# Performance work log

Measured on AMD Instinct MI355X. Metric: run time of the kernel, lower is better.

The kernel has to match this reference:

```python
import jax, jax.numpy as jnp
import numpy as np

D_MODEL = 1024
NUM_HEADS = 16
D_HEAD = 64
N_CTX = 2048
BATCH = 4
NEG_INF = -1e10  # matches torch masked_fill value


def setup_inputs() -> dict:
    key = jax.random.key(0)
    k1, k2, k3, k4, k5 = jax.random.split(key, 5)
    s = 1.0 / np.sqrt(D_MODEL).astype(np.float32)
    x = jax.random.normal(k1, (BATCH, N_CTX, D_MODEL), dtype=jnp.float32)
    W_K = jax.random.normal(k2, (NUM_HEADS, D_HEAD, D_MODEL), dtype=jnp.float32) * s
    W_Q = jax.random.normal(k3, (NUM_HEADS, D_HEAD, D_MODEL), dtype=jnp.float32) * s
    W_V = jax.random.normal(k4, (NUM_HEADS, D_HEAD, D_MODEL), dtype=jnp.float32) * s
    W_O = jax.random.normal(k5, (D_MODEL, NUM_HEADS * D_HEAD), dtype=jnp.float32) * s
    return {"x": x, "W_K": W_K, "W_Q": W_Q, "W_V": W_V, "W_O": W_O}


def reference(x, W_K, W_Q, W_V, W_O):
    b, q_len, d_model = x.shape
    d_head = W_K.shape[1]
    # projections: b=batch, p=pos, d=d_model, i=head, h=d_head
    K = jnp.einsum('bpd,ihd->biph', x, W_K)
    Q = jnp.einsum('bpd,ihd->biph', x, W_Q)
    V = jnp.einsum('bpd,ihd->biph', x, W_V)
    # scores[b, i, q, p] = Q[b,i,q,:] . K[b,i,p,:]
    scores = jnp.einsum('biph,biqh->biqp', K, Q)
    mask = jnp.tril(jnp.ones((q_len, q_len), dtype=bool))
    # NOTE: original masks with -1e10 BEFORE dividing by sqrt(d_head)
    scores = jnp.where(mask[None, None, :, :], scores, NEG_INF)
    attn = jax.nn.softmax(scores / np.sqrt(d_head).astype(np.float32), axis=-1)
    z = jnp.einsum('biph,biqp->biqh', V, attn)
    z_flat = jnp.transpose(z, (0, 2, 1, 3)).reshape(b, q_len, -1)  # b q (i h)
    out = jnp.einsum('bqf,df->bqd', z_flat, W_O)
    return out
```

## Files before the change

kernel.cpp:

```cpp
#include <hip/hip_runtime.h>
#include <hip/hip_bf16.h>


typedef short short8 __attribute__((ext_vector_type(8)));
typedef float f32x4 __attribute__((ext_vector_type(4)));

#define MFMA16(a, b, c) __builtin_amdgcn_mfma_f32_16x16x32_bf16((a), (b), (c), 0, 0, 0)

static __device__ __forceinline__ ushort f2bf(float f) {
  union { __hip_bfloat16 h; ushort u; } cv;
  cv.h = __float2bfloat16(f);
  return cv.u;
}

static __device__ __forceinline__ float fexp2(float x) {
#if __has_builtin(__builtin_amdgcn_exp2f)
  return __builtin_amdgcn_exp2f(x);
#else
  return __expf(x * 0.69314718056f);
#endif
}

static __device__ __forceinline__ void block_sync_lds() {
  asm volatile("s_waitcnt lgkmcnt(0)" ::: "memory");
  __builtin_amdgcn_s_barrier();
  __builtin_amdgcn_sched_barrier(0);
}

static __device__ __forceinline__ void block_sync_full() {
  asm volatile("s_waitcnt vmcnt(0) lgkmcnt(0)" ::: "memory");
  __builtin_amdgcn_s_barrier();
  __builtin_amdgcn_sched_barrier(0);
}

static __device__ __forceinline__ void store_out(float* p, float v) { *p = v; }
static __device__ __forceinline__ void store_out(__hip_bfloat16* p, float v) {
  *p = __float2bfloat16(v);
}

__global__ __launch_bounds__(256) void convert_all_kernel(
    const float* __restrict__ wq, const float* __restrict__ wk,
    const float* __restrict__ wv, const float* __restrict__ wo,
    const float* __restrict__ x, ushort* __restrict__ wqkv,
    ushort* __restrict__ wob, ushort* __restrict__ xb) {
  constexpr int W4 = 262144;
  constexpr size_t WSZ = (size_t)1024 * 1024;
  const int i = blockIdx.x * blockDim.x + threadIdx.x;
  const float* src;
  ushort* dst;
  int j;
  if (i < 2 * W4) {
    if (i < W4)      { src = wq; dst = wqkv;           j = i; }
    else             { src = wk; dst = wqkv + WSZ;     j = i - W4; }
  } else if (i < 4 * W4) {
    if (i < 3 * W4)  { src = wv; dst = wqkv + 2 * WSZ; j = i - 2 * W4; }
    else             { src = wo; dst = wob;            j = i - 3 * W4; }
  } else {
    src = x; dst = xb; j = i - 4 * W4;
  }
  const float4 v = ((const float4*)src)[j];
  ushort4 o;
  o.x = f2bf(v.x); o.y = f2bf(v.y); o.z = f2bf(v.z); o.w = f2bf(v.w);
  ((ushort4*)dst)[j] = o;
}

template <typename OUT_T>
__global__ __launch_bounds__(256) void gemm_kernel(
    const ushort* __restrict__ A, int lda, const ushort* __restrict__ B, int ldb,
    OUT_T* __restrict__ C, int ldc, int K, int cpx) {
  __shared__ __align__(16) ushort As[128 * 64];
  __shared__ __align__(16) ushort Bs[128 * 64];
  const int tid = threadIdx.x;
  const int wave = tid >> 6, lane = tid & 63;
  const int lm = lane & 15, quad = lane >> 4;

  const int id = blockIdx.x;
  const int local = id >> 3;
  const int nt = (id & 7) * cpx + local % cpx;
  const int mt = local / cpx;
  const size_t m0 = (size_t)mt * 128;
  const size_t n0 = (size_t)nt * 128;

  const int rl = lane >> 3;
  const int cs = (lane & 7) ^ rl;
  const int fsw = lm & 7;

  f32x4 acc[4][4] = {};
  for (int k0 = 0; k0 < K; k0 += 64) {
    __syncthreads();
#pragma unroll
    for (int j = 0; j < 4; ++j) {
      const int ch = wave * 4 + j;
      const ushort* gb = B + (n0 + ch * 8 + rl) * (size_t)ldb + k0 + cs * 8;
      __builtin_amdgcn_global_load_lds(
          (const __attribute__((address_space(1))) void*)gb,
          (__attribute__((address_space(3))) void*)(Bs + ch * 512), 16, 0, 0);
      const ushort* ga = A + (m0 + ch * 8 + rl) * (size_t)lda + k0 + cs * 8;
      __builtin_amdgcn_global_load_lds(
          (const __attribute__((address_space(1))) void*)ga,
          (__attribute__((address_space(3))) void*)(As + ch * 512), 16, 0, 0);
    }
    __syncthreads();

    const int wm = (wave >> 1) * 64, wn = (wave & 1) * 64;
#pragma unroll
    for (int ks = 0; ks < 2; ++ks) {
      short8 a[4], b[4];
#pragma unroll
      for (int i = 0; i < 4; ++i)
        a[i] = *(const short8*)(As + (wm + i * 16 + lm) * 64 +
                                ((((ks * 4 + quad) ^ fsw) & 7) << 3));
#pragma unroll
      for (int j = 0; j < 4; ++j)
        b[j] = *(const short8*)(Bs + (wn + j * 16 + lm) * 64 +
                                ((((ks * 4 + quad) ^ fsw) & 7) << 3));
#pragma unroll
      for (int i = 0; i < 4; ++i)
#pragma unroll
        for (int j = 0; j < 4; ++j)
          acc[i][j] = MFMA16(a[i], b[j], acc[i][j]);
    }
  }

  const int wm = (wave >> 1) * 64, wn = (wave & 1) * 64;
  const int rq = quad * 4;
#pragma unroll
  for (int i = 0; i < 4; ++i)
#pragma unroll
    for (int j = 0; j < 4; ++j)
#pragma unroll
      for (int r = 0; r < 4; ++r)
        store_out(&C[(m0 + wm + i * 16 + rq + r) * (size_t)ldc + n0 + wn + j * 16 + lm],
                  acc[i][j][r]);
}

static __device__ __forceinline__ void vt_write8(ushort* vtbuf, int h0, int hsw,
                                                 int p, const short8& v) {
  const int pc = (p >> 3) ^ hsw;
  ushort* row = vtbuf + h0 * 64 + (p & 7);
#pragma unroll
  for (int u = 0; u < 8; ++u)
    row[u * 64 + (((pc ^ u) & 7) << 3)] = ((const ushort*)&v)[u];
}

static __device__ __forceinline__ void stage_k(const ushort* kglob, int pbase,
                                               ushort* kbuf, int wave, int lane) {
  const int rl = lane >> 3;
  const int c = (lane & 7) ^ rl;
#pragma unroll
  for (int j = 0; j < 2; ++j) {
    const int ch = wave * 2 + j;
    const ushort* src = kglob + (size_t)(pbase + ch * 8 + rl) * 3072 + c * 8;
    __builtin_amdgcn_global_load_lds(
        (const __attribute__((address_space(1))) void*)src,
        (__attribute__((address_space(3))) void*)(kbuf + ch * 512), 16, 0, 0);
  }
}

__global__ __launch_bounds__(256) void flash4_kernel(ushort* __restrict__ QKV) {
  constexpr int LD = 3072;
  __shared__ __align__(16) ushort vt[2][64 * 64];
  __shared__ __align__(16) ushort kt[2][64 * 64];
  __shared__ __align__(16) ushort pbuf[4][16 * 64];

  const int id = blockIdx.x;
  const int g = (id & 7) * 8 + ((id >> 3) & 7);
  const int m = id >> 6;
  const int head = g & 15;
  const int b = g >> 4;

  const int tid = threadIdx.x;
  const int wave = tid >> 6, lane = tid & 63;
  const int lm = lane & 15, quad = lane >> 4;

  const size_t qcol = (size_t)b * 2048 * LD + head * 64;
  const size_t vcol = qcol + 2048;
  const ushort* kglob = QKV + qcol + 1024;

  const int h0 = (tid & 7) * 8;
  const int hsw = tid & 7;
  const int plb = tid >> 3;
  const int psw = lm & 7;
  const int ksw = lm & 7;

  constexpr float CSC = 0.180336880f;

  for (int pass = 0; pass < 2; ++pass) {
    const int qbi = pass ? 31 - m : m;
    const int qrow = qbi * 64 + wave * 16;
    const int qg = qrow + lm;
    const int nt = qbi + 1;

    const ushort* qp = QKV + qcol + (size_t)(qrow + lm) * LD;
    short8 qa0 = *(const short8*)(qp + quad * 8);
    short8 qa1 = *(const short8*)(qp + 32 + quad * 8);

    f32x4 accz[4] = {};
    float l_l = 0.f;

    block_sync_lds();

    stage_k(kglob, 0, kt[0], wave, lane);
#pragma unroll
    for (int rr = 0; rr < 2; ++rr) {
      const int p = plb + rr * 32;
      short8 v = *(const short8*)(QKV + vcol + (size_t)p * LD + h0);
      vt_write8(vt[0], h0, hsw, p, v);
    }

    for (int it = 0; it < nt; ++it) {
      const int p0 = it * 64;
      block_sync_full();

      short8 ka[4], kb[4];
      const ushort* kbuf = kt[it & 1];
#pragma unroll
      for (int s = 0; s < 4; ++s) {
        const ushort* kr = kbuf + (s * 16 + lm) * 64;
        ka[s] = *(const short8*)(kr + (((quad ^ ksw) & 7) << 3));
        kb[s] = *(const short8*)(kr + ((((quad + 4) ^ ksw) & 7) << 3));
      }

      const bool more = (it + 1 < nt);
      short8 nv0, nv1;
      if (more) {
        nv0 = *(const short8*)(QKV + vcol + (size_t)(p0 + 64 + plb) * LD + h0);
        nv1 = *(const short8*)(QKV + vcol + (size_t)(p0 + 96 + plb) * LD + h0);
        stage_k(kglob, p0 + 64, kt[(it + 1) & 1], wave, lane);
      }

      f32x4 t4[4];
#pragma unroll
      for (int s = 0; s < 4; ++s) {
        f32x4 t = {0.f, 0.f, 0.f, 0.f};
        t = MFMA16(ka[s], qa0, t);
        t = MFMA16(kb[s], qa1, t);
        t4[s] = t;
      }

      float ps[4][4];
      if (it != nt - 1) {
#pragma unroll
        for (int s = 0; s < 4; ++s) {
#pragma unroll
          for (int r = 0; r < 4; ++r)
            ps[s][r] = fexp2(t4[s][r] * CSC);
          l_l += (ps[s][0] + ps[s][1]) + (ps[s][2] + ps[s][3]);
        }
      } else {
#pragma unroll
        for (int s = 0; s < 4; ++s) {
#pragma unroll
          for (int r = 0; r < 4; ++r) {
            const int pg = p0 + s * 16 + quad * 4 + r;
            const float e = fexp2(t4[s][r] * CSC);
            ps[s][r] = (pg > qg) ? 0.f : e;
          }
          l_l += (ps[s][0] + ps[s][1]) + (ps[s][2] + ps[s][3]);
        }
      }

      ushort* pw = pbuf[wave] + lm * 64;
#pragma unroll
      for (int s = 0; s < 4; ++s) {
        uint2 pk;
        pk.x = (uint)f2bf(ps[s][0]) | ((uint)f2bf(ps[s][1]) << 16);
        pk.y = (uint)f2bf(ps[s][2]) | ((uint)f2bf(ps[s][3]) << 16);
        *(uint2*)(pw + ((((2 * s + (quad >> 1)) ^ psw) & 7) << 3) +
                  ((quad & 1) << 2)) = pk;
      }

      const ushort* vbuf = vt[it & 1];
#pragma unroll
      for (int kc = 0; kc < 2; ++kc) {
        short8 pa = *(const short8*)(pw + ((((kc * 4 + quad) ^ psw) & 7) << 3));
#pragma unroll
        for (int c = 0; c < 4; ++c) {
          const int hrow = c * 16 + lm;
          const int fh = ((hrow >> 3) ^ hrow) & 7;
          short8 vb = *(const short8*)(
              vbuf + hrow * 64 + ((((4 * kc + quad) ^ fh) & 7) << 3));
          accz[c] = MFMA16(pa, vb, accz[c]);
        }
      }

      if (more) {
        ushort* nbuf = vt[(it + 1) & 1];
        vt_write8(nbuf, h0, hsw, plb, nv0);
        vt_write8(nbuf, h0, hsw, plb + 32, nv1);
      }
    }

    float lt = l_l;
    lt += __shfl_xor(lt, 16, 64);
    lt += __shfl_xor(lt, 32, 64);
#pragma unroll
    for (int r = 0; r < 4; ++r) {
      const float lr = __shfl(lt, quad * 4 + r, 64);
      const float inv = 1.f / lr;
#pragma unroll
      for (int c = 0; c < 4; ++c)
        QKV[qcol + (size_t)(qrow + quad * 4 + r) * LD + c * 16 + lm] =
            f2bf(accz[c][r] * inv);
    }
  }
}

extern "C" void kernel_launch(void* const* d_in, const int* in_sizes, int n_in,
                              void* d_out, int out_size, void* d_ws, size_t ws_size,
                              hipStream_t stream) {
  (void)in_sizes; (void)n_in; (void)out_size; (void)ws_size;
  const float* x  = (const float*)d_in[0];
  const float* wk = (const float*)d_in[1];
  const float* wq = (const float*)d_in[2];
  const float* wv = (const float*)d_in[3];
  const float* wo = (const float*)d_in[4];
  float* out = (float*)d_out;

  const size_t WSZ = (size_t)1024 * 1024;
  ushort* wqkv_b = (ushort*)d_ws;
  ushort* wo_b = wqkv_b + 3 * WSZ;
  ushort* QKV = wo_b + WSZ;
  ushort* xb = (ushort*)d_out;

  convert_all_kernel<<<12288, 256, 0, stream>>>(wq, wk, wv, wo, x,
                                                wqkv_b, wo_b, xb);

  gemm_kernel<__hip_bfloat16><<<1536, 256, 0, stream>>>(
      xb, 1024, wqkv_b, 1024, (__hip_bfloat16*)QKV, 3072, 1024, 3);

  flash4_kernel<<<1024, 256, 0, stream>>>(QKV);

  gemm_kernel<float><<<512, 256, 0, stream>>>(
      QKV, 3072, wo_b, 1024, out, 1024, 1024, 1);
}
```

Before: 262.3 us.

## Fuse paired causal query tiles into one KV sweep sharing K/V staging

Each block used to handle query tiles m and 31-m in two separate passes, loading K/V twice. Now both tiles are processed in one loop over KV tiles: the low tile is active only for the first m+1 iterations, and every staged K/V tile is reused by both. The block-to-tile mapping also changes to interleave small and large m values across consecutive block ids. This removes the repeated K/V loads and pass prologues, at the cost of more live registers (two accumulator sets and two Q fragments), which may lower occupancy.

```diff
diff --git a/kernel.cpp b/kernel.cpp
--- a/kernel.cpp
+++ b/kernel.cpp
@@ -164,8 +164,9 @@
   __shared__ __align__(16) ushort pbuf[4][16 * 64];
 
   const int id = blockIdx.x;
-  const int g = (id & 7) * 8 + ((id >> 3) & 7);
-  const int m = id >> 6;
+  const int pk = (id >> 3) & 15;
+  const int g = (id & 7) * 8 + (id >> 7);
+  const int m = (pk & 1) ? 15 - (pk >> 1) : (pk >> 1);
   const int head = g & 15;
   const int b = g >> 4;
 
@@ -185,67 +186,83 @@
 
   constexpr float CSC = 0.180336880f;
 
-  for (int pass = 0; pass < 2; ++pass) {
-    const int qbi = pass ? 31 - m : m;
-    const int qrow = qbi * 64 + wave * 16;
-    const int qg = qrow + lm;
-    const int nt = qbi + 1;
-
-    const ushort* qp = QKV + qcol + (size_t)(qrow + lm) * LD;
-    short8 qa0 = *(const short8*)(qp + quad * 8);
-    short8 qa1 = *(const short8*)(qp + 32 + quad * 8);
-
-    f32x4 accz[4] = {};
-    float l_l = 0.f;
-
-    block_sync_lds();
-
-    stage_k(kglob, 0, kt[0], wave, lane);
-#pragma unroll
-    for (int rr = 0; rr < 2; ++rr) {
-      const int p = plb + rr * 32;
-      short8 v = *(const short8*)(QKV + vcol + (size_t)p * LD + h0);
-      vt_write8(vt[0], h0, hsw, p, v);
-    }
-
-    for (int it = 0; it < nt; ++it) {
-      const int p0 = it * 64;
-      block_sync_full();
-
-      short8 ka[4], kb[4];
-      const ushort* kbuf = kt[it & 1];
-#pragma unroll
-      for (int s = 0; s < 4; ++s) {
-        const ushort* kr = kbuf + (s * 16 + lm) * 64;
-        ka[s] = *(const short8*)(kr + (((quad ^ ksw) & 7) << 3));
-        kb[s] = *(const short8*)(kr + ((((quad + 4) ^ ksw) & 7) << 3));
-      }
-
-      const bool more = (it + 1 < nt);
-      short8 nv0, nv1;
-      if (more) {
-        nv0 = *(const short8*)(QKV + vcol + (size_t)(p0 + 64 + plb) * LD + h0);
-        nv1 = *(const short8*)(QKV + vcol + (size_t)(p0 + 96 + plb) * LD + h0);
-        stage_k(kglob, p0 + 64, kt[(it + 1) & 1], wave, lane);
-      }
-
-      f32x4 t4[4];
+  const int qrowA = m * 64 + wave * 16;
+  const int qrowB = (31 - m) * 64 + wave * 16;
+  const int qgA = qrowA + lm;
+  const int qgB = qrowB + lm;
+  const int np = 32 - m;
+
+  const ushort* qpA = QKV + qcol + (size_t)(qrowA + lm) * LD;
+  short8 qaA0 = *(const short8*)(qpA + quad * 8);
+  short8 qaA1 = *(const short8*)(qpA + 32 + quad * 8);
+  const ushort* qpB = QKV + qcol + (size_t)(qrowB + lm) * LD;
+  short8 qaB0 = *(const short8*)(qpB + quad * 8);
+  short8 qaB1 = *(const short8*)(qpB + 32 + quad * 8);
+
+  f32x4 acczA[4] = {}, acczB[4] = {};
+  float llA = 0.f, llB = 0.f;
+
+  stage_k(kglob, 0, kt[0], wave, lane);
+#pragma unroll
+  for (int rr = 0; rr < 2; ++rr) {
+    const int p = plb + rr * 32;
+    short8 v = *(const short8*)(QKV + vcol + (size_t)p * LD + h0);
+    vt_write8(vt[0], h0, hsw, p, v);
+  }
+
+  for (int it = 0; it < np; ++it) {
+    const int p0 = it * 64;
+    block_sync_full();
+
+    short8 ka[4], kb[4];
+    const ushort* kbuf = kt[it & 1];
+#pragma unroll
+    for (int s = 0; s < 4; ++s) {
+      const ushort* kr = kbuf + (s * 16 + lm) * 64;
+      ka[s] = *(const short8*)(kr + (((quad ^ ksw) & 7) << 3));
+      kb[s] = *(const short8*)(kr + ((((quad + 4) ^ ksw) & 7) << 3));
+    }
+
+    const bool more = (it + 1 < np);
+    short8 nv0, nv1;
+    if (more) {
+      nv0 = *(const short8*)(QKV + vcol + (size_t)(p0 + 64 + plb) * LD + h0);
+      nv1 = *(const short8*)(QKV + vcol + (size_t)(p0 + 96 + plb) * LD + h0);
+      stage_k(kglob, p0 + 64, kt[(it + 1) & 1], wave, lane);
+    }
+
+    const bool actA = (it <= m);
+
+    f32x4 t4A[4], t4B[4];
+    if (actA) {
 #pragma unroll
       for (int s = 0; s < 4; ++s) {
         f32x4 t = {0.f, 0.f, 0.f, 0.f};
-        t = MFMA16(ka[s], qa0, t);
-        t = MFMA16(kb[s], qa1, t);
-        t4[s] = t;
-      }
-
+        t = MFMA16(ka[s], qaA0, t);
+        t = MFMA16(kb[s], qaA1, t);
+        t4A[s] = t;
+      }
+    }
+#pragma unroll
+    for (int s = 0; s < 4; ++s) {
+      f32x4 t = {0.f, 0.f, 0.f, 0.f};
+      t = MFMA16(ka[s], qaB0, t);
+      t = MFMA16(kb[s], qaB1, t);
+      t4B[s] = t;
+    }
+
+    const ushort* vbuf = vt[it & 1];
+    ushort* pw = pbuf[wave] + lm * 64;
+
+    if (actA) {
       float ps[4][4];
-      if (it != nt - 1) {
+      if (it != m) {
 #pragma unroll
         for (int s = 0; s < 4; ++s) {
 #pragma unroll
           for (int r = 0; r < 4; ++r)
-            ps[s][r] = fexp2(t4[s][r] * CSC);
-          l_l += (ps[s][0] + ps[s][1]) + (ps[s][2] + ps[s][3]);
+            ps[s][r] = fexp2(t4A[s][r] * CSC);
+          llA += (ps[s][0] + ps[s][1]) + (ps[s][2] + ps[s][3]);
         }
       } else {
 #pragma unroll
@@ -253,24 +270,20 @@
 #pragma unroll
           for (int r = 0; r < 4; ++r) {
             const int pg = p0 + s * 16 + quad * 4 + r;
-            const float e = fexp2(t4[s][r] * CSC);
-            ps[s][r] = (pg > qg) ? 0.f : e;
+            const float e = fexp2(t4A[s][r] * CSC);
+            ps[s][r] = (pg > qgA) ? 0.f : e;
           }
-          l_l += (ps[s][0] + ps[s][1]) + (ps[s][2] + ps[s][3]);
-        }
-      }
-
-      ushort* pw = pbuf[wave] + lm * 64;
+          llA += (ps[s][0] + ps[s][1]) + (ps[s][2] + ps[s][3]);
+        }
+      }
 #pragma unroll
       for (int s = 0; s < 4; ++s) {
-        uint2 pk;
-        pk.x = (uint)f2bf(ps[s][0]) | ((uint)f2bf(ps[s][1]) << 16);
-        pk.y = (uint)f2bf(ps[s][2]) | ((uint)f2bf(ps[s][3]) << 16);
+        uint2 pkv;
+        pkv.x = (uint)f2bf(ps[s][0]) | ((uint)f2bf(ps[s][1]) << 16);
+        pkv.y = (uint)f2bf(ps[s][2]) | ((uint)f2bf(ps[s][3]) << 16);
         *(uint2*)(pw + ((((2 * s + (quad >> 1)) ^ psw) & 7) << 3) +
-                  ((quad & 1) << 2)) = pk;
-      }
-
-      const ushort* vbuf = vt[it & 1];
+                  ((quad & 1) << 2)) = pkv;
+      }
 #pragma unroll
       for (int kc = 0; kc < 2; ++kc) {
         short8 pa = *(const short8*)(pw + ((((kc * 4 + quad) ^ psw) & 7) << 3));
@@ -280,18 +293,64 @@
           const int fh = ((hrow >> 3) ^ hrow) & 7;
           short8 vb = *(const short8*)(
               vbuf + hrow * 64 + ((((4 * kc + quad) ^ fh) & 7) << 3));
-          accz[c] = MFMA16(pa, vb, accz[c]);
-        }
-      }
-
-      if (more) {
-        ushort* nbuf = vt[(it + 1) & 1];
-        vt_write8(nbuf, h0, hsw, plb, nv0);
-        vt_write8(nbuf, h0, hsw, plb + 32, nv1);
-      }
-    }
-
-    float lt = l_l;
+          acczA[c] = MFMA16(pa, vb, acczA[c]);
+        }
+      }
+    }
+
+    {
+      float ps[4][4];
+      if (it != np - 1) {
+#pragma unroll
+        for (int s = 0; s < 4; ++s) {
+#pragma unroll
+          for (int r = 0; r < 4; ++r)
+            ps[s][r] = fexp2(t4B[s][r] * CSC);
+          llB += (ps[s][0] + ps[s][1]) + (ps[s][2] + ps[s][3]);
+        }
+      } else {
+#pragma unroll
+        for (int s = 0; s < 4; ++s) {
+#pragma unroll
+          for (int r = 0; r < 4; ++r) {
+            const int pg = p0 + s * 16 + quad * 4 + r;
+            const float e = fexp2(t4B[s][r] * CSC);
+            ps[s][r] = (pg > qgB) ? 0.f : e;
+          }
+          llB += (ps[s][0] + ps[s][1]) + (ps[s][2] + ps[s][3]);
+        }
+      }
+#pragma unroll
+      for (int s = 0; s < 4; ++s) {
+        uint2 pkv;
+        pkv.x = (uint)f2bf(ps[s][0]) | ((uint)f2bf(ps[s][1]) << 16);
+        pkv.y = (uint)f2bf(ps[s][2]) | ((uint)f2bf(ps[s][3]) << 16);
+        *(uint2*)(pw + ((((2 * s + (quad >> 1)) ^ psw) & 7) << 3) +
+                  ((quad & 1) << 2)) = pkv;
+      }
+#pragma unroll
+      for (int kc = 0; kc < 2; ++kc) {
+        short8 pa = *(const short8*)(pw + ((((kc * 4 + quad) ^ psw) & 7) << 3));
+#pragma unroll
+        for (int c = 0; c < 4; ++c) {
+          const int hrow = c * 16 + lm;
+          const int fh = ((hrow >> 3) ^ hrow) & 7;
+          short8 vb = *(const short8*)(
+              vbuf + hrow * 64 + ((((4 * kc + quad) ^ fh) & 7) << 3));
+          acczB[c] = MFMA16(pa, vb, acczB[c]);
+        }
+      }
+    }
+
+    if (more) {
+      ushort* nbuf = vt[(it + 1) & 1];
+      vt_write8(nbuf, h0, hsw, plb, nv0);
+      vt_write8(nbuf, h0, hsw, plb + 32, nv1);
+    }
+  }
+
+  {
+    float lt = llA;
     lt += __shfl_xor(lt, 16, 64);
     lt += __shfl_xor(lt, 32, 64);
 #pragma unroll
@@ -300,8 +359,22 @@
       const float inv = 1.f / lr;
 #pragma unroll
       for (int c = 0; c < 4; ++c)
-        QKV[qcol + (size_t)(qrow + quad * 4 + r) * LD + c * 16 + lm] =
-            f2bf(accz[c][r] * inv);
+        QKV[qcol + (size_t)(qrowA + quad * 4 + r) * LD + c * 16 + lm] =
+            f2bf(acczA[c][r] * inv);
+    }
+  }
+  {
+    float lt = llB;
+    lt += __shfl_xor(lt, 16, 64);
+    lt += __shfl_xor(lt, 32, 64);
+#pragma unroll
+    for (int r = 0; r < 4; ++r) {
+      const float lr = __shfl(lt, quad * 4 + r, 64);
+      const float inv = 1.f / lr;
+#pragma unroll
+      for (int c = 0; c < 4; ++c)
+        QKV[qcol + (size_t)(qrowB + quad * 4 + r) * LD + c * 16 + lm] =
+            f2bf(acczB[c][r] * inv);
     }
   }
 }
```

New measurement: 275.9 us. 1.05x slower.
